# Optimization experiments

Hardware: AMD Instinct MI355X
Metric: run time of the kernel (lower is better)

The kernel has to match this reference:

```python
import jax, jax.numpy as jnp
import numpy as np

B, C, H, W = 32, 64, 128, 128
RADIUS = 30


def _dw(x, w, dil, pad):
    # depthwise conv, NCHW, groups = C
    return jax.lax.conv_general_dilated(
        x, w, window_strides=(1, 1), padding=[(pad, pad), (pad, pad)],
        rhs_dilation=(dil, dil),
        dimension_numbers=('NCHW', 'OIHW', 'NCHW'),
        feature_group_count=x.shape[1])


def _pw(x, w):
    # 1x1 conv: w is [out_ch, in_ch]
    return jnp.einsum('bchw,oc->bohw', x, w)


def _aff(x, s, b):
    # folded BatchNorm (inference): per-channel scale + bias
    return x * s[None, :, None, None] + b[None, :, None, None]


def setup_inputs() -> dict:
    key = jax.random.key(0)
    ks = iter(jax.random.split(key, 40))
    nk = lambda: next(ks)
    rn = lambda shape, sc=0.1: jax.random.normal(nk(), shape, jnp.float32) * sc
    ru = lambda shape: jax.random.uniform(nk(), shape, jnp.float32, minval=0.5, maxval=1.5)
    d = {'x': jax.random.normal(nk(), (B, C, H, W), jnp.float32)}
    d['dws_dw'] = rn((C, 1, 3, 3)); d['dws_s1'] = ru((C,)); d['dws_b1'] = rn((C,))
    d['dws_pw'] = rn((C, C)); d['dws_s2'] = ru((C,)); d['dws_b2'] = rn((C,))
    kern = {1: 1, 2: 3, 3: 3, 4: 3}
    for i in (1, 2, 3, 4):
        d[f'dw{i}_w'] = rn((C, 1, kern[i], kern[i]))
        d[f'dw{i}_s'] = ru((C,)); d[f'dw{i}_b'] = rn((C,))
        d[f'pw{i}_w'] = rn((C // 4, C)); d[f'pw{i}_s'] = ru((C // 4,)); d[f'pw{i}_b'] = rn((C // 4,))
    d['conv_w'] = rn((1, C)); d['conv_s'] = ru((1,)); d['conv_b'] = rn((1,))
    d['radius'] = RADIUS
    return d


def reference(x, dws_dw, dws_s1, dws_b1, dws_pw, dws_s2, dws_b2,
              dw1_w, dw1_s, dw1_b, pw1_w, pw1_s, pw1_b,
              dw2_w, dw2_s, dw2_b, pw2_w, pw2_s, pw2_b,
              dw3_w, dw3_s, dw3_b, pw3_w, pw3_s, pw3_b,
              dw4_w, dw4_s, dw4_b, pw4_w, pw4_s, pw4_b,
              conv_w, conv_s, conv_b, radius):
    rows, cols = x.shape[-2], x.shape[-1]
    # vectorized radial mask (original builds this with a Python double loop)
    ii = jnp.arange(rows, dtype=jnp.float32)[:, None]
    jj = jnp.arange(cols, dtype=jnp.float32)[None, :]
    dis = jnp.sqrt((ii - rows / 2) ** 2 + (jj - rows / 2) ** 2)  # note: imageSize=rows for both axes, as in original
    mask = (dis < radius).astype(x.dtype)
    # FFT high-pass filter
    xf = jnp.fft.fftshift(jnp.fft.fft2(x, axes=(-2, -1)), axes=(-2, -1))
    hf = xf * (1.0 - mask)
    x_h = jnp.abs(jnp.fft.ifft2(jnp.fft.ifftshift(hf, axes=(-2, -1)), axes=(-2, -1))).astype(x.dtype)
    # DWSConv: depthwise 3x3 + BN + ReLU, then pointwise + BN + ReLU
    e = jax.nn.relu(_aff(_dw(x_h, dws_dw, 1, 1), dws_s1, dws_b1))
    e = jax.nn.relu(_aff(_pw(e, dws_pw), dws_s2, dws_b2))
    skip = e

    def branch(t, dw_w, dw_s, dw_b, pw_w, pw_s, pw_b, dil, pad):
        # DWConv (depthwise + BN + ReLU) then BasicConv2d 1x1 (conv + BN)
        t = jax.nn.relu(_aff(_dw(t, dw_w, dil, pad), dw_s, dw_b))
        return _aff(_pw(t, pw_w), pw_s, pw_b)

    em = jnp.concatenate([
        branch(e, dw1_w, dw1_s, dw1_b, pw1_w, pw1_s, pw1_b, 1, 0),
        branch(e, dw2_w, dw2_s, dw2_b, pw2_w, pw2_s, pw2_b, 1, 1),
        branch(e, dw3_w, dw3_s, dw3_b, pw3_w, pw3_s, pw3_b, 3, 3),
        branch(e, dw4_w, dw4_s, dw4_b, pw4_w, pw4_s, pw4_b, 5, 5),
    ], axis=1) + skip
    edge = jax.nn.relu(_aff(_pw(em, conv_w), conv_s, conv_b))  # [B,1,H,W]
    return _aff(_pw(x + edge, conv_w), conv_s, conv_b)  # shared self.conv applied again
```

## Files before the change

kernel.cpp:

```cpp
#include <hip/hip_runtime.h>


__device__ __forceinline__ float2 cmul(float2 a, float2 b) {
  return make_float2(a.x * b.x - a.y * b.y, a.x * b.y + a.y * b.x);
}
__device__ __forceinline__ float2 cadd(float2 a, float2 b) {
  return make_float2(a.x + b.x, a.y + b.y);
}
__device__ __forceinline__ float2 csub(float2 a, float2 b) {
  return make_float2(a.x - b.x, a.y - b.y);
}
__device__ __forceinline__ float2 conjf2(float2 a) {
  return make_float2(a.x, -a.y);
}

__device__ __forceinline__ int swz(int r, int c) {
  return (r << 7) | (c ^ (r & 31));
}

__device__ __forceinline__ void bf3_fwd(float2 x[8], float2 t0, float2 t1,
                                        float2 t2, float2 t3, float2 tp0,
                                        float2 tp1, float2 tpp) {
  float2 y0 = cadd(x[0], x[4]), y4 = cmul(csub(x[0], x[4]), t0);
  float2 y1 = cadd(x[1], x[5]), y5 = cmul(csub(x[1], x[5]), t1);
  float2 y2 = cadd(x[2], x[6]), y6 = cmul(csub(x[2], x[6]), t2);
  float2 y3 = cadd(x[3], x[7]), y7 = cmul(csub(x[3], x[7]), t3);
  float2 z0 = cadd(y0, y2), z2 = cmul(csub(y0, y2), tp0);
  float2 z1 = cadd(y1, y3), z3 = cmul(csub(y1, y3), tp1);
  float2 z4 = cadd(y4, y6), z6 = cmul(csub(y4, y6), tp0);
  float2 z5 = cadd(y5, y7), z7 = cmul(csub(y5, y7), tp1);
  x[0] = cadd(z0, z1); x[1] = cmul(csub(z0, z1), tpp);
  x[2] = cadd(z2, z3); x[3] = cmul(csub(z2, z3), tpp);
  x[4] = cadd(z4, z5); x[5] = cmul(csub(z4, z5), tpp);
  x[6] = cadd(z6, z7); x[7] = cmul(csub(z6, z7), tpp);
}

__device__ __forceinline__ void bf3_inv(float2 x[8], float2 w0, float2 w10,
                                        float2 w11, float2 w20, float2 w21,
                                        float2 w22, float2 w23) {
  float2 t;
  t = cmul(x[1], w0); float2 y0 = cadd(x[0], t), y1 = csub(x[0], t);
  t = cmul(x[3], w0); float2 y2 = cadd(x[2], t), y3 = csub(x[2], t);
  t = cmul(x[5], w0); float2 y4 = cadd(x[4], t), y5 = csub(x[4], t);
  t = cmul(x[7], w0); float2 y6 = cadd(x[6], t), y7 = csub(x[6], t);
  t = cmul(y2, w10); float2 z0 = cadd(y0, t), z2 = csub(y0, t);
  t = cmul(y3, w11); float2 z1 = cadd(y1, t), z3 = csub(y1, t);
  t = cmul(y6, w10); float2 z4 = cadd(y4, t), z6 = csub(y4, t);
  t = cmul(y7, w11); float2 z5 = cadd(y5, t), z7 = csub(y5, t);
  t = cmul(z4, w20); x[0] = cadd(z0, t); x[4] = csub(z0, t);
  t = cmul(z5, w21); x[1] = cadd(z1, t); x[5] = csub(z1, t);
  t = cmul(z6, w22); x[2] = cadd(z2, t); x[6] = csub(z2, t);
  t = cmul(z7, w23); x[3] = cadd(z3, t); x[7] = csub(z3, t);
}

template <bool COL, int S>
__device__ __forceinline__ void fwd_tri(float2* img, const float2* tw,
                                        int tid) {
  constexpr int m4 = 1 << (S - 2);
#pragma unroll
  for (int k = 0; k < 2; ++k) {
    int g = tid + (k << 10);
    int line = COL ? (g & 127) : (g >> 4);
    int gidx = COL ? (g >> 7) : (g & 15);
    int q = gidx >> (S - 2);
    int j = gidx & (m4 - 1);
    int off0 = (q << (S + 1)) + j;
    int ad[8];
    float2 x[8];
#pragma unroll
    for (int i = 0; i < 8; ++i) {
      int el = off0 + i * m4;
      ad[i] = COL ? swz(el, line) : swz(line, el);
      x[i] = img[ad[i]];
    }
    bf3_fwd(x, tw[j << (6 - S)], tw[(j + m4) << (6 - S)],
            tw[(j + 2 * m4) << (6 - S)], tw[(j + 3 * m4) << (6 - S)],
            tw[j << (7 - S)], tw[(j + m4) << (7 - S)], tw[j << (8 - S)]);
#pragma unroll
    for (int i = 0; i < 8; ++i) img[ad[i]] = x[i];
  }
  __syncthreads();
}

__device__ __forceinline__ void fwd_rows6_g(const float* __restrict__ p0,
                                            const float* __restrict__ p1,
                                            float2* img, const float2* tw,
                                            int tid) {
#pragma unroll
  for (int k = 0; k < 2; ++k) {
    int g = tid + (k << 10);
    int line = g >> 4;
    int j = g & 15;
    float2 x[8];
#pragma unroll
    for (int i = 0; i < 8; ++i) {
      int a = (line << 7) + j + (i << 4);
      x[i] = make_float2(p0[a], p1[a]);
    }
    bf3_fwd(x, tw[j], tw[j + 16], tw[j + 32], tw[j + 48], tw[j << 1],
            tw[(j + 16) << 1], tw[j << 2]);
#pragma unroll
    for (int i = 0; i < 8; ++i) img[swz(line, j + (i << 4))] = x[i];
  }
  __syncthreads();
}

__device__ __forceinline__ void fwd_last_rows(float2* img, int tid) {
#pragma unroll
  for (int k = 0; k < 8; ++k) {
    int g = tid + (k << 10);
    int line = g >> 6;
    int pr = g & 63;
    int e0 = pr << 1;
    int a0 = swz(line, e0), a1 = swz(line, e0 + 1);
    float2 a = img[a0], b = img[a1];
    img[a0] = cadd(a, b);
    img[a1] = csub(a, b);
  }
  __syncthreads();
}

__device__ __forceinline__ void fwd_last_cols_mask(float2* img, int tid) {
#pragma unroll
  for (int k = 0; k < 8; ++k) {
    int g = tid + (k << 10);
    int line = g & 127;
    int pr = g >> 7;
    int e0 = pr << 1;
    int a0 = swz(e0, line), a1 = swz(e0 + 1, line);
    float2 a = img[a0], b = img[a1];
    float2 s = cadd(a, b), d = csub(a, b);
    int v = __brev((unsigned)line) >> 25;
    int dv = v - ((v >= 64) << 7);
    int u0 = __brev((unsigned)e0) >> 25;
    int du0 = u0 - ((u0 >= 64) << 7);
    int u1 = __brev((unsigned)(e0 + 1)) >> 25;
    int du1 = u1 - ((u1 >= 64) << 7);
    int dvv = dv * dv;
    img[a0] = (du0 * du0 + dvv < 900) ? make_float2(0.f, 0.f) : s;
    img[a1] = (du1 * du1 + dvv < 900) ? make_float2(0.f, 0.f) : d;
  }
  __syncthreads();
}

template <bool COL, int S>
__device__ __forceinline__ void inv_tri(float2* img, const float2* tw,
                                        int tid) {
  constexpr int m = 1 << S;
#pragma unroll
  for (int k = 0; k < 2; ++k) {
    int g = tid + (k << 10);
    int line = COL ? (g & 127) : (g >> 4);
    int gidx = COL ? (g >> 7) : (g & 15);
    int q = gidx >> S;
    int j = gidx & (m - 1);
    int off0 = (q << (S + 3)) + j;
    int ad[8];
    float2 x[8];
#pragma unroll
    for (int i = 0; i < 8; ++i) {
      int el = off0 + i * m;
      ad[i] = COL ? swz(el, line) : swz(line, el);
      x[i] = img[ad[i]];
    }
    bf3_inv(x, conjf2(tw[j << (6 - S)]), conjf2(tw[j << (5 - S)]),
            conjf2(tw[(j + m) << (5 - S)]), conjf2(tw[j << (4 - S)]),
            conjf2(tw[(j + m) << (4 - S)]), conjf2(tw[(j + 2 * m) << (4 - S)]),
            conjf2(tw[(j + 3 * m) << (4 - S)]));
#pragma unroll
    for (int i = 0; i < 8; ++i) img[ad[i]] = x[i];
  }
  __syncthreads();
}

__device__ __forceinline__ void inv_last_cols(float2* img, const float2* tw,
                                              int tid) {
#pragma unroll
  for (int k = 0; k < 8; ++k) {
    int g = tid + (k << 10);
    int line = g & 127;
    int j = g >> 7;
    int a0 = swz(j, line), a1 = swz(j + 64, line);
    float2 a = img[a0], b = img[a1];
    float2 t = cmul(b, conjf2(tw[j]));
    img[a0] = cadd(a, t);
    img[a1] = csub(a, t);
  }
  __syncthreads();
}

__device__ __forceinline__ void inv_last_rows_store(const float2* img,
                                                    const float2* tw,
                                                    float* __restrict__ q0,
                                                    float* __restrict__ q1,
                                                    int tid) {
#pragma unroll
  for (int k = 0; k < 8; ++k) {
    int g = tid + (k << 10);
    int line = g >> 6;
    int j = g & 63;
    float2 a = img[swz(line, j)], b = img[swz(line, j + 64)];
    float2 t = cmul(b, conjf2(tw[j]));
    float2 o0 = cadd(a, t), o1 = csub(a, t);
    int p = (line << 7) + j;
    q0[p] = fabsf(o0.x) * 6.103515625e-05f;
    q1[p] = fabsf(o0.y) * 6.103515625e-05f;
    q0[p + 64] = fabsf(o1.x) * 6.103515625e-05f;
    q1[p + 64] = fabsf(o1.y) * 6.103515625e-05f;
  }
}

__global__ __launch_bounds__(1024) void k_fft_hp(const float* __restrict__ x,
                                                 float* __restrict__ xh) {
  __shared__ float2 img[16384];
  __shared__ float2 tw[64];
  const int tid = threadIdx.x;
  const size_t base = (size_t)blockIdx.x * 32768;
  const float* p0 = x + base;
  const float* p1 = p0 + 16384;

  if (tid < 64) {
    float ang = -0.04908738521234052f * (float)tid;
    tw[tid] = make_float2(cosf(ang), sinf(ang));
  }
  __syncthreads();

  fwd_rows6_g(p0, p1, img, tw, tid);
  fwd_tri<false, 3>(img, tw, tid);
  fwd_last_rows(img, tid);
  fwd_tri<true, 6>(img, tw, tid);
  fwd_tri<true, 3>(img, tw, tid);
  fwd_last_cols_mask(img, tid);

  inv_tri<true, 0>(img, tw, tid);
  inv_tri<true, 3>(img, tw, tid);
  inv_last_cols(img, tw, tid);
  inv_tri<false, 0>(img, tw, tid);
  inv_tri<false, 3>(img, tw, tid);
  inv_last_rows_store(img, tw, xh + base, xh + base + 16384, tid);
}

#define DWS_LD(chunk)                                                          \
  {                                                                            \
    _Pragma("unroll") for (int k2 = 0; k2 < 7; ++k2) {                         \
      int idx = t + (k2 << 8);                                                 \
      float4 v = make_float4(0.f, 0.f, 0.f, 0.f);                              \
      if (idx < 1600) {                                                        \
        int c = idx / 100;                                                     \
        int rem = idx - c * 100;                                               \
        int row = rem / 10;                                                    \
        int g = rem - row * 10;                                                \
        int grow = gy0 + row;                                                  \
        int gcol = gxb + (g << 2);                                             \
        if (grow >= 0 && grow < 128 && gcol >= 0 && gcol <= 124)               \
          v = *(const float4*)(xh + (((size_t)bb * 64 + ((chunk) << 4) + c)    \
                                     << 14) + (grow << 7) + gcol);             \
      }                                                                        \
      sg[k2] = v;                                                              \
    }                                                                          \
  }

#define DWS_ST()                                                               \
  {                                                                            \
    _Pragma("unroll") for (int k2 = 0; k2 < 7; ++k2) {                         \
      int idx = t + (k2 << 8);                                                 \
      if (idx < 1600) {                                                        \
        int c = idx / 100;                                                     \
        int rem = idx - c * 100;                                               \
        *(float4*)&inT[c][rem << 2] = sg[k2];                                  \
      }                                                                        \
    }                                                                          \
  }

__global__ __launch_bounds__(256) void k_dws(
    const float* __restrict__ xh, float* __restrict__ e,
    const float* __restrict__ dw_w, const float* __restrict__ s1,
    const float* __restrict__ b1, const float* __restrict__ pw_w,
    const float* __restrict__ s2, const float* __restrict__ b2) {
  __shared__ float inT[16][400];

  const int t = threadIdx.x;
  const int bb = blockIdx.x >> 6;
  const int ty = (blockIdx.x >> 2) & 15;
  const int tx = blockIdx.x & 3;
  const int r = t >> 5;
  const int x = t & 31;

  const int gy0 = (ty << 3) - 1;
  const int gxb = (tx << 5) - 4;

  float acc[64];
#pragma unroll
  for (int o = 0; o < 64; ++o) acc[o] = 0.f;

  float4 sg[7];
  DWS_LD(0);

#pragma unroll 1
  for (int chunk = 0; chunk < 4; ++chunk) {
    DWS_ST();
    __syncthreads();
    if (chunk < 3) DWS_LD(chunk + 1);

    float dwv[16];
#pragma unroll
    for (int c = 0; c < 16; ++c) {
      const int cg = (chunk << 4) + c;
      const float* wp = dw_w + cg * 9;
      const float* p = &inT[c][r * 40 + x + 3];
      float s = wp[0] * p[0];
      s = fmaf(wp[1], p[1], s);
      s = fmaf(wp[2], p[2], s);
      s = fmaf(wp[3], p[40], s);
      s = fmaf(wp[4], p[41], s);
      s = fmaf(wp[5], p[42], s);
      s = fmaf(wp[6], p[80], s);
      s = fmaf(wp[7], p[81], s);
      s = fmaf(wp[8], p[82], s);
      dwv[c] = fmaxf(fmaf(s, s1[cg], b1[cg]), 0.f);
    }

#pragma unroll
    for (int o = 0; o < 64; ++o) {
      const float* w = pw_w + (o << 6) + (chunk << 4);
#pragma unroll
      for (int c = 0; c < 16; ++c) acc[o] = fmaf(w[c], dwv[c], acc[o]);
    }
    __syncthreads();
  }

  const int gy = (ty << 3) + r;
  const int gx = (tx << 5) + x;
#pragma unroll
  for (int o = 0; o < 64; ++o) {
    float ev = fmaxf(fmaf(acc[o], s2[o], b2[o]), 0.f);
    e[(((size_t)bb * 64 + o) << 14) + (gy << 7) + gx] = ev;
  }
}

struct BrParams {
  const float *dw1w, *dw1s, *dw1b, *pw1w, *pw1s, *pw1b;
  const float *dw2w, *dw2s, *dw2b, *pw2w, *pw2s, *pw2b;
  const float *dw3w, *dw3s, *dw3b, *pw3w, *pw3s, *pw3b;
  const float *dw4w, *dw4s, *dw4b, *pw4w, *pw4s, *pw4b;
};

#define STAGE_LD(chunk)                                                        \
  {                                                                            \
    _Pragma("unroll") for (int k2 = 0; k2 < 9; ++k2) {                         \
      int idx = t + (k2 << 8);                                                 \
      float4 v = make_float4(0.f, 0.f, 0.f, 0.f);                              \
      if (idx < 2080) {                                                        \
        int jj = idx >= 1040;                                                  \
        int rem = idx - (jj ? 1040 : 0);                                       \
        int row = rem / 40;                                                    \
        int col4 = rem - row * 40;                                             \
        int grow = gy0 + row;                                                  \
        if (grow >= 0 && grow < 128 && col4 >= 2 && col4 < 34) {               \
          int cg = ((chunk) << 1) + jj;                                        \
          v = *(const float4*)(eg + (((size_t)bb * 64 + cg) << 14) +           \
                               (grow << 7) + (col4 << 2) - 8);                 \
        }                                                                      \
      }                                                                        \
      sg[k2] = v;                                                              \
    }                                                                          \
  }

#define STAGE_ST(pbuf)                                                         \
  {                                                                            \
    _Pragma("unroll") for (int k2 = 0; k2 < 9; ++k2) {                         \
      int idx = t + (k2 << 8);                                                 \
      if (idx < 2080) {                                                        \
        int jj = idx >= 1040;                                                  \
        int rem = idx - (jj ? 1040 : 0);                                       \
        int row = rem / 40;                                                    \
        int col4 = rem - row * 40;                                             \
        *(float4*)&sE[pbuf][jj * 4160 + row * 160 +                            \
                            ((col4 ^ (col4 >> 3)) << 2)] = sg[k2];             \
      }                                                                        \
    }                                                                          \
  }

__global__ __launch_bounds__(256, 1) void k_edge_final(
    const float* __restrict__ eg, const float* __restrict__ xg,
    float* __restrict__ out, BrParams P, const float* __restrict__ cw,
    const float* __restrict__ cs, const float* __restrict__ cb) {
  __shared__ float sE[2][8320];
  __shared__ float w2r[768], w3r[768], w4r[768];
  __shared__ float chp[1024];
  __shared__ float dwSs[4][64], dwBs[4][64], gs[4][64];
  __shared__ float dw1Ws[64], cws[64];
  __shared__ float pss[4][16], pbs[4][16];
  __shared__ float KbS, swS;

  const int t = threadIdx.x;
  const int bb = blockIdx.x >> 3;
  const int ty = blockIdx.x & 7;
  const int r = t >> 4;
  const int x0 = (t & 15) << 3;
  const int gy = (ty << 4) + r;
  const int gy0 = (ty << 4) - 5;

  for (int i = t; i < 576; i += 256) {
    int row = i / 9, q = i - row * 9;
    w2r[row * 12 + q] = P.dw2w[i];
    w3r[row * 12 + q] = P.dw3w[i];
    w4r[row * 12 + q] = P.dw4w[i];
  }
  if (t < 64) {
    dw1Ws[t] = P.dw1w[t];
    cws[t] = cw[t];
    dwSs[0][t] = P.dw1s[t]; dwBs[0][t] = P.dw1b[t];
    dwSs[1][t] = P.dw2s[t]; dwBs[1][t] = P.dw2b[t];
    dwSs[2][t] = P.dw3s[t]; dwBs[2][t] = P.dw3b[t];
    dwSs[3][t] = P.dw4s[t]; dwBs[3][t] = P.dw4b[t];
  }
  if (t < 16) {
    pss[0][t] = P.pw1s[t]; pbs[0][t] = P.pw1b[t];
    pss[1][t] = P.pw2s[t]; pbs[1][t] = P.pw2b[t];
    pss[2][t] = P.pw3s[t]; pbs[2][t] = P.pw3b[t];
    pss[3][t] = P.pw4s[t]; pbs[3][t] = P.pw4b[t];
  }
  __syncthreads();
  {
    const int q = t >> 6, c = t & 63;
    const float* pwW = (q == 0) ? P.pw1w : (q == 1) ? P.pw2w
                        : (q == 2) ? P.pw3w : P.pw4w;
    float gv = 0.f;
#pragma unroll
    for (int o = 0; o < 16; ++o)
      gv = fmaf(cws[(q << 4) + o] * pss[q][o], pwW[(o << 6) + c], gv);
    gs[q][c] = gv;
  }
  if (t == 0) {
    float kb = 0.f, sw = 0.f;
#pragma unroll
    for (int i = 0; i < 64; ++i) {
      kb = fmaf(cws[i], pbs[i >> 4][i & 15], kb);
      sw += cws[i];
    }
    KbS = kb;
    swS = sw;
  }
  __syncthreads();
  if (t < 64) {
    float* cp = &chp[t << 4];
    cp[0] = dw1Ws[t];  cp[1] = cws[t];
    cp[2] = dwSs[0][t]; cp[3] = dwBs[0][t];
    cp[4] = dwSs[1][t]; cp[5] = dwBs[1][t];
    cp[6] = dwSs[2][t]; cp[7] = dwBs[2][t];
    cp[8] = dwSs[3][t]; cp[9] = dwBs[3][t];
    cp[10] = gs[0][t]; cp[11] = gs[1][t];
    cp[12] = gs[2][t]; cp[13] = gs[3][t];
  }

  const int gbase = (t & 15) << 1;
  int so[6];
#pragma unroll
  for (int k = 0; k < 6; ++k) {
    int g = gbase + k;
    so[k] = (g ^ (g >> 3)) << 2;
  }

  float4 sg[9];
  STAGE_LD(0);
  STAGE_ST(0);
  STAGE_LD(1);
  __syncthreads();

  float eacc[8], es8[8], sxa[8];
#pragma unroll
  for (int k = 0; k < 8; ++k) { eacc[k] = 0.f; es8[k] = 0.f; sxa[k] = 0.f; }

  const float csv = cs[0], cbv = cb[0];

#pragma unroll 1
  for (int c = 0; c < 32; ++c) {
    if (c + 1 < 32) STAGE_ST((c + 1) & 1);
    if (c + 2 < 32) STAGE_LD(c + 2);
    const float* bp = &sE[c & 1][0];
#pragma unroll 1
    for (int j = 0; j < 2; ++j) {
      const int cg = (c << 1) + j;
      const float* ldc = bp + j * 4160;
      const float* xp = xg + (((size_t)bb * 64 + cg) << 14) + (gy << 7) + x0;
      float xv[8];
      *(float4*)&xv[0] = *(const float4*)xp;
      *(float4*)&xv[4] = *(const float4*)(xp + 4);
      const float4 Q0 = *(const float4*)&chp[cg << 4];
      const float4 Q1 = *(const float4*)&chp[(cg << 4) + 4];
      const float4 Q2 = *(const float4*)&chp[(cg << 4) + 8];
      const float4 Q3 = *(const float4*)&chp[(cg << 4) + 12];

      float cr[24];
      const float* rowc = ldc + (r + 5) * 160;
      *(float4*)&cr[0] = *(const float4*)(rowc + so[0]);
      *(float4*)&cr[4] = *(const float4*)(rowc + so[1]);
      *(float4*)&cr[8] = *(const float4*)(rowc + so[2]);
      *(float4*)&cr[12] = *(const float4*)(rowc + so[3]);
      *(float4*)&cr[16] = *(const float4*)(rowc + so[4]);
      *(float4*)&cr[20] = *(const float4*)(rowc + so[5]);

#pragma unroll
      for (int k = 0; k < 8; ++k) {
        float ec = cr[8 + k];
        es8[k] = fmaf(Q0.y, ec, es8[k]);
        float d0 = fmaxf(fmaf(ec * Q0.x, Q0.z, Q0.w), 0.f);
        eacc[k] = fmaf(Q2.z, d0, eacc[k]);
      }
      float mm[24], pp[24];
      {
        const float4 w2a = *(const float4*)&w2r[cg * 12];
        const float4 w2b = *(const float4*)&w2r[cg * 12 + 4];
        const float4 w2c = *(const float4*)&w2r[cg * 12 + 8];
        const float* rm = ldc + (r + 4) * 160;
        const float* rp = ldc + (r + 6) * 160;
        *(float4*)&mm[0] = *(const float4*)(rm + so[1]);
        *(float4*)&mm[4] = *(const float4*)(rm + so[2]);
        *(float4*)&mm[8] = *(const float4*)(rm + so[3]);
        *(float4*)&mm[12] = *(const float4*)(rm + so[4]);
        *(float4*)&pp[0] = *(const float4*)(rp + so[1]);
        *(float4*)&pp[4] = *(const float4*)(rp + so[2]);
        *(float4*)&pp[8] = *(const float4*)(rp + so[3]);
        *(float4*)&pp[12] = *(const float4*)(rp + so[4]);
#pragma unroll
        for (int k = 0; k < 8; ++k) {
          float s = w2a.x * mm[3 + k];
          s = fmaf(w2a.y, mm[4 + k], s);
          s = fmaf(w2a.z, mm[5 + k], s);
          s = fmaf(w2a.w, cr[7 + k], s);
          s = fmaf(w2b.x, cr[8 + k], s);
          s = fmaf(w2b.y, cr[9 + k], s);
          s = fmaf(w2b.z, pp[3 + k], s);
          s = fmaf(w2b.w, pp[4 + k], s);
          s = fmaf(w2c.x, pp[5 + k], s);
          float d1 = fmaxf(fmaf(s, Q1.x, Q1.y), 0.f);
          eacc[k] = fmaf(Q2.w, d1, eacc[k]);
        }
      }
      {
        const float4 w3a = *(const float4*)&w3r[cg * 12];
        const float4 w3b = *(const float4*)&w3r[cg * 12 + 4];
        const float4 w3c = *(const float4*)&w3r[cg * 12 + 8];
        const float* rm = ldc + (r + 2) * 160;
        const float* rp = ldc + (r + 8) * 160;
        *(float4*)&mm[0] = *(const float4*)(rm + so[1]);
        *(float4*)&mm[4] = *(const float4*)(rm + so[2]);
        *(float4*)&mm[8] = *(const float4*)(rm + so[3]);
        *(float4*)&mm[12] = *(const float4*)(rm + so[4]);
        *(float4*)&pp[0] = *(const float4*)(rp + so[1]);
        *(float4*)&pp[4] = *(const float4*)(rp + so[2]);
        *(float4*)&pp[8] = *(const float4*)(rp + so[3]);
        *(float4*)&pp[12] = *(const float4*)(rp + so[4]);
#pragma unroll
        for (int k = 0; k < 8; ++k) {
          float s = w3a.x * mm[1 + k];
          s = fmaf(w3a.y, mm[4 + k], s);
          s = fmaf(w3a.z, mm[7 + k], s);
          s = fmaf(w3a.w, cr[5 + k], s);
          s = fmaf(w3b.x, cr[8 + k], s);
          s = fmaf(w3b.y, cr[11 + k], s);
          s = fmaf(w3b.z, pp[1 + k], s);
          s = fmaf(w3b.w, pp[4 + k], s);
          s = fmaf(w3c.x, pp[7 + k], s);
          float d2 = fmaxf(fmaf(s, Q1.z, Q1.w), 0.f);
          eacc[k] = fmaf(Q3.x, d2, eacc[k]);
        }
      }
      {
        const float4 w4a = *(const float4*)&w4r[cg * 12];
        const float4 w4b = *(const float4*)&w4r[cg * 12 + 4];
        const float4 w4c = *(const float4*)&w4r[cg * 12 + 8];
        const float* rm = ldc + (r + 0) * 160;
        const float* rp = ldc + (r + 10) * 160;
        *(float4*)&mm[0] = *(const float4*)(rm + so[0]);
        *(float4*)&mm[4] = *(const float4*)(rm + so[1]);
        *(float4*)&mm[8] = *(const float4*)(rm + so[2]);
        *(float4*)&mm[12] = *(const float4*)(rm + so[3]);
        *(float4*)&mm[16] = *(const float4*)(rm + so[4]);
        *(float4*)&mm[20] = *(const float4*)(rm + so[5]);
        *(float4*)&pp[0] = *(const float4*)(rp + so[0]);
        *(float4*)&pp[4] = *(const float4*)(rp + so[1]);
        *(float4*)&pp[8] = *(const float4*)(rp + so[2]);
        *(float4*)&pp[12] = *(const float4*)(rp + so[3]);
        *(float4*)&pp[16] = *(const float4*)(rp + so[4]);
        *(float4*)&pp[20] = *(const float4*)(rp + so[5]);
#pragma unroll
        for (int k = 0; k < 8; ++k) {
          float s = w4a.x * mm[3 + k];
          s = fmaf(w4a.y, mm[8 + k], s);
          s = fmaf(w4a.z, mm[13 + k], s);
          s = fmaf(w4a.w, cr[3 + k], s);
          s = fmaf(w4b.x, cr[8 + k], s);
          s = fmaf(w4b.y, cr[13 + k], s);
          s = fmaf(w4b.z, pp[3 + k], s);
          s = fmaf(w4b.w, pp[8 + k], s);
          s = fmaf(w4c.x, pp[13 + k], s);
          float d3 = fmaxf(fmaf(s, Q2.x, Q2.y), 0.f);
          eacc[k] = fmaf(Q3.y, d3, eacc[k]);
        }
      }
#pragma unroll
      for (int k = 0; k < 8; ++k) sxa[k] = fmaf(Q0.y, xv[k], sxa[k]);
    }
    __syncthreads();
  }

  const float kb = KbS, sw = swS;
  float ov[8];
#pragma unroll
  for (int k = 0; k < 8; ++k) {
    float ee = fmaxf(fmaf(eacc[k] + kb + es8[k], csv, cbv), 0.f);
    ov[k] = fmaf(sxa[k] + ee * sw, csv, cbv);
  }
  float* op = out + ((size_t)bb << 14) + (gy << 7) + x0;
  *(float4*)op = *(float4*)&ov[0];
  *(float4*)(op + 4) = *(float4*)&ov[4];
}

extern "C" void kernel_launch(void* const* d_in, const int* in_sizes, int n_in,
                              void* d_out, int out_size, void* d_ws,
                              size_t ws_size, hipStream_t stream) {
  (void)in_sizes; (void)n_in; (void)out_size; (void)ws_size;
  const float* x = (const float*)d_in[0];
  const float* dws_dw = (const float*)d_in[1];
  const float* dws_s1 = (const float*)d_in[2];
  const float* dws_b1 = (const float*)d_in[3];
  const float* dws_pw = (const float*)d_in[4];
  const float* dws_s2 = (const float*)d_in[5];
  const float* dws_b2 = (const float*)d_in[6];
  BrParams P;
  P.dw1w = (const float*)d_in[7];  P.dw1s = (const float*)d_in[8];
  P.dw1b = (const float*)d_in[9];  P.pw1w = (const float*)d_in[10];
  P.pw1s = (const float*)d_in[11]; P.pw1b = (const float*)d_in[12];
  P.dw2w = (const float*)d_in[13]; P.dw2s = (const float*)d_in[14];
  P.dw2b = (const float*)d_in[15]; P.pw2w = (const float*)d_in[16];
  P.pw2s = (const float*)d_in[17]; P.pw2b = (const float*)d_in[18];
  P.dw3w = (const float*)d_in[19]; P.dw3s = (const float*)d_in[20];
  P.dw3b = (const float*)d_in[21]; P.pw3w = (const float*)d_in[22];
  P.pw3s = (const float*)d_in[23]; P.pw3b = (const float*)d_in[24];
  P.dw4w = (const float*)d_in[25]; P.dw4s = (const float*)d_in[26];
  P.dw4b = (const float*)d_in[27]; P.pw4w = (const float*)d_in[28];
  P.pw4s = (const float*)d_in[29]; P.pw4b = (const float*)d_in[30];
  const float* conv_w = (const float*)d_in[31];
  const float* conv_s = (const float*)d_in[32];
  const float* conv_b = (const float*)d_in[33];

  float* xh = (float*)d_ws;
  float* e = xh + (size_t)33554432;

  hipLaunchKernelGGL(k_fft_hp, dim3(1024), dim3(1024), 0, stream, x, xh);
  hipLaunchKernelGGL(k_dws, dim3(2048), dim3(256), 0, stream, xh, e, dws_dw,
                     dws_s1, dws_b1, dws_pw, dws_s2, dws_b2);
  hipLaunchKernelGGL(k_edge_final, dim3(256), dim3(256), 0, stream, e, x,
                     (float*)d_out, P, conv_w, conv_s, conv_b);
}
```

Before: 714.6 us.

## Stage depthwise and edge tiles via direct global-to-LDS async loads

Replaces the register-staged global loads plus LDS stores in the DWS and edge-final kernels with __builtin_amdgcn_global_load_lds, which copies 16 bytes directly into double-buffered shared memory. Out-of-bounds halo elements are loaded from clamped addresses and then overwritten with zeros by a fix-up pass. The offsets are precomputed per thread, and the edge kernel's swizzle is folded into the source addresses. The goal is to free the staging registers and the VGPR-to-LDS traffic, and the occupancy hint on the edge kernel is dropped. The risk is added syncs, and there is no visible wait on the async load counter before the data is consumed.

```diff
diff --git a/kernel.cpp b/kernel.cpp
--- a/kernel.cpp
+++ b/kernel.cpp
@@ -12,6 +12,12 @@
 }
 __device__ __forceinline__ float2 conjf2(float2 a) {
   return make_float2(a.x, -a.y);
+}
+
+__device__ __forceinline__ void gload16(const float* g, void* l) {
+  __builtin_amdgcn_global_load_lds(
+      (const __attribute__((address_space(1))) void*)g,
+      (__attribute__((address_space(3))) void*)l, 16, 0, 0);
 }
 
 __device__ __forceinline__ int swz(int r, int c) {
@@ -240,35 +246,22 @@
   inv_last_rows_store(img, tw, xh + base, xh + base + 16384, tid);
 }
 
-#define DWS_LD(chunk)                                                          \
+#define DWS_G(chunk, buf)                                                      \
   {                                                                            \
     _Pragma("unroll") for (int k2 = 0; k2 < 7; ++k2) {                         \
       int idx = t + (k2 << 8);                                                 \
-      float4 v = make_float4(0.f, 0.f, 0.f, 0.f);                              \
-      if (idx < 1600) {                                                        \
-        int c = idx / 100;                                                     \
-        int rem = idx - c * 100;                                               \
-        int row = rem / 10;                                                    \
-        int g = rem - row * 10;                                                \
-        int grow = gy0 + row;                                                  \
-        int gcol = gxb + (g << 2);                                             \
-        if (grow >= 0 && grow < 128 && gcol >= 0 && gcol <= 124)               \
-          v = *(const float4*)(xh + (((size_t)bb * 64 + ((chunk) << 4) + c)    \
-                                     << 14) + (grow << 7) + gcol);             \
-      }                                                                        \
-      sg[k2] = v;                                                              \
+      if (idx < 1600)                                                          \
+        gload16(xh + xbase + (size_t)(chunk) * 262144 + offs[k2],              \
+                &inT[buf][idx << 2]);                                          \
     }                                                                          \
   }
 
-#define DWS_ST()                                                               \
+#define DWS_FIX(buf)                                                           \
   {                                                                            \
     _Pragma("unroll") for (int k2 = 0; k2 < 7; ++k2) {                         \
-      int idx = t + (k2 << 8);                                                 \
-      if (idx < 1600) {                                                        \
-        int c = idx / 100;                                                     \
-        int rem = idx - c * 100;                                               \
-        *(float4*)&inT[c][rem << 2] = sg[k2];                                  \
-      }                                                                        \
+      if ((fixm >> k2) & 1)                                                    \
+        *(float4*)&inT[buf][(t + (k2 << 8)) << 2] =                            \
+            make_float4(0.f, 0.f, 0.f, 0.f);                                   \
     }                                                                          \
   }
 
@@ -277,7 +270,7 @@
     const float* __restrict__ dw_w, const float* __restrict__ s1,
     const float* __restrict__ b1, const float* __restrict__ pw_w,
     const float* __restrict__ s2, const float* __restrict__ b2) {
-  __shared__ float inT[16][400];
+  __shared__ __align__(16) float inT[2][6400];
 
   const int t = threadIdx.x;
   const int bb = blockIdx.x >> 6;
@@ -288,26 +281,52 @@
 
   const int gy0 = (ty << 3) - 1;
   const int gxb = (tx << 5) - 4;
+  const size_t xbase = (size_t)bb << 20;
+  const bool bfix = (ty == 0) | (ty == 15) | (tx == 0) | (tx == 3);
+
+  unsigned fixm = 0;
+  int offs[7];
+#pragma unroll
+  for (int k2 = 0; k2 < 7; ++k2) {
+    int idx = t + (k2 << 8);
+    offs[k2] = 0;
+    if (idx < 1600) {
+      int c = idx / 100;
+      int rem = idx - c * 100;
+      int row = rem / 10;
+      int g = rem - row * 10;
+      int grow = gy0 + row;
+      int gcol = gxb + (g << 2);
+      if ((grow < 0) | (grow > 127) | (gcol < 0) | (gcol > 124))
+        fixm |= (1u << k2);
+      int grc = grow < 0 ? 0 : (grow > 127 ? 127 : grow);
+      int gcc = gcol < 0 ? 0 : (gcol > 124 ? 124 : gcol);
+      offs[k2] = (c << 14) + (grc << 7) + gcc;
+    }
+  }
 
   float acc[64];
 #pragma unroll
   for (int o = 0; o < 64; ++o) acc[o] = 0.f;
 
-  float4 sg[7];
-  DWS_LD(0);
+  DWS_G(0, 0);
+  __syncthreads();
 
 #pragma unroll 1
   for (int chunk = 0; chunk < 4; ++chunk) {
-    DWS_ST();
-    __syncthreads();
-    if (chunk < 3) DWS_LD(chunk + 1);
+    if (bfix) {
+      DWS_FIX(chunk & 1);
+      __syncthreads();
+    }
+    if (chunk < 3) DWS_G(chunk + 1, (chunk + 1) & 1);
+    const float* base = &inT[chunk & 1][0];
 
     float dwv[16];
 #pragma unroll
     for (int c = 0; c < 16; ++c) {
       const int cg = (chunk << 4) + c;
       const float* wp = dw_w + cg * 9;
-      const float* p = &inT[c][r * 40 + x + 3];
+      const float* p = base + c * 400 + r * 40 + x + 3;
       float s = wp[0] * p[0];
       s = fmaf(wp[1], p[1], s);
       s = fmaf(wp[2], p[2], s);
@@ -345,47 +364,30 @@
   const float *dw4w, *dw4s, *dw4b, *pw4w, *pw4s, *pw4b;
 };
 
-#define STAGE_LD(chunk)                                                        \
+#define EDGE_G(chunk, buf)                                                     \
   {                                                                            \
     _Pragma("unroll") for (int k2 = 0; k2 < 9; ++k2) {                         \
       int idx = t + (k2 << 8);                                                 \
-      float4 v = make_float4(0.f, 0.f, 0.f, 0.f);                              \
-      if (idx < 2080) {                                                        \
-        int jj = idx >= 1040;                                                  \
-        int rem = idx - (jj ? 1040 : 0);                                       \
-        int row = rem / 40;                                                    \
-        int col4 = rem - row * 40;                                             \
-        int grow = gy0 + row;                                                  \
-        if (grow >= 0 && grow < 128 && col4 >= 2 && col4 < 34) {               \
-          int cg = ((chunk) << 1) + jj;                                        \
-          v = *(const float4*)(eg + (((size_t)bb * 64 + cg) << 14) +           \
-                               (grow << 7) + (col4 << 2) - 8);                 \
-        }                                                                      \
-      }                                                                        \
-      sg[k2] = v;                                                              \
+      if (idx < 2080)                                                          \
+        gload16(eg + ebase + (size_t)(chunk) * 32768 + eoffs[k2],              \
+                &sE[buf][idx << 2]);                                           \
     }                                                                          \
   }
 
-#define STAGE_ST(pbuf)                                                         \
+#define EDGE_FIX(buf)                                                          \
   {                                                                            \
     _Pragma("unroll") for (int k2 = 0; k2 < 9; ++k2) {                         \
-      int idx = t + (k2 << 8);                                                 \
-      if (idx < 2080) {                                                        \
-        int jj = idx >= 1040;                                                  \
-        int rem = idx - (jj ? 1040 : 0);                                       \
-        int row = rem / 40;                                                    \
-        int col4 = rem - row * 40;                                             \
-        *(float4*)&sE[pbuf][jj * 4160 + row * 160 +                            \
-                            ((col4 ^ (col4 >> 3)) << 2)] = sg[k2];             \
-      }                                                                        \
+      if ((fixm >> k2) & 1)                                                    \
+        *(float4*)&sE[buf][(t + (k2 << 8)) << 2] =                             \
+            make_float4(0.f, 0.f, 0.f, 0.f);                                   \
     }                                                                          \
   }
 
-__global__ __launch_bounds__(256, 1) void k_edge_final(
+__global__ __launch_bounds__(256) void k_edge_final(
     const float* __restrict__ eg, const float* __restrict__ xg,
     float* __restrict__ out, BrParams P, const float* __restrict__ cw,
     const float* __restrict__ cs, const float* __restrict__ cb) {
-  __shared__ float sE[2][8320];
+  __shared__ __align__(16) float sE[2][8320];
   __shared__ float w2r[768], w3r[768], w4r[768];
   __shared__ float chp[1024];
   __shared__ float dwSs[4][64], dwBs[4][64], gs[4][64];
@@ -400,6 +402,7 @@
   const int x0 = (t & 15) << 3;
   const int gy = (ty << 4) + r;
   const int gy0 = (ty << 4) - 5;
+  const size_t ebase = (size_t)bb << 20;
 
   for (int i = t; i < 576; i += 256) {
     int row = i / 9, q = i - row * 9;
@@ -454,6 +457,26 @@
     cp[12] = gs[2][t]; cp[13] = gs[3][t];
   }
 
+  unsigned fixm = 0;
+  int eoffs[9];
+#pragma unroll
+  for (int k2 = 0; k2 < 9; ++k2) {
+    int idx = t + (k2 << 8);
+    eoffs[k2] = 0;
+    if (idx < 2080) {
+      int jj = idx >= 1040;
+      int rem = idx - (jj ? 1040 : 0);
+      int row = rem / 40;
+      int q = rem - row * 40;
+      int s = q ^ (q >> 3);
+      int grow = gy0 + row;
+      if ((grow < 0) | (grow > 127) | (s < 2) | (s > 33)) fixm |= (1u << k2);
+      int grc = grow < 0 ? 0 : (grow > 127 ? 127 : grow);
+      int sc = s < 2 ? 2 : (s > 33 ? 33 : s);
+      eoffs[k2] = (jj << 14) + (grc << 7) + (sc << 2) - 8;
+    }
+  }
+
   const int gbase = (t & 15) << 1;
   int so[6];
 #pragma unroll
@@ -462,10 +485,7 @@
     so[k] = (g ^ (g >> 3)) << 2;
   }
 
-  float4 sg[9];
-  STAGE_LD(0);
-  STAGE_ST(0);
-  STAGE_LD(1);
+  EDGE_G(0, 0);
   __syncthreads();
 
   float eacc[8], es8[8], sxa[8];
@@ -476,8 +496,9 @@
 
 #pragma unroll 1
   for (int c = 0; c < 32; ++c) {
-    if (c + 1 < 32) STAGE_ST((c + 1) & 1);
-    if (c + 2 < 32) STAGE_LD(c + 2);
+    EDGE_FIX(c & 1);
+    __syncthreads();
+    if (c + 1 < 32) EDGE_G(c + 1, (c + 1) & 1);
     const float* bp = &sE[c & 1][0];
 #pragma unroll 1
     for (int j = 0; j < 2; ++j) {
```

Measured after the change: 671.2 us. -6.1%, faster.
